# Performance work log

Measured on AMD Instinct MI355X. Metric: run time of the kernel, lower is better.

Reference implementation:

```python
import jax, jax.numpy as jnp
import numpy as np

B, P, A, V = 16, 4096, 32, 778


def _pairwise_dist(x, y):
    # x: (B, N, 3), y: (B, M, 3) -> (B, N, M) euclidean distances (torch.cdist p=2)
    d2 = (jnp.sum(x * x, -1)[:, :, None]
          + jnp.sum(y * y, -1)[:, None, :]
          - 2.0 * jnp.einsum('bnd,bmd->bnm', x, y))
    return jnp.sqrt(jnp.maximum(d2, 1e-12))


def setup_inputs() -> dict:
    key = jax.random.key(0)
    ks = jax.random.split(key, 8)
    verts = jax.random.normal(ks[0], (B, V, 3), jnp.float32) * 0.1
    anchors = jax.random.normal(ks[1], (B, A, 3), jnp.float32) * 0.1
    # choir columns: [bps_dist, dx, dy, dz, anchor_dist, anchor_idx]
    bps_d = jax.random.uniform(ks[2], (B, P, 1), jnp.float32)
    deltas = jax.random.normal(ks[3], (B, P, 3), jnp.float32) * 0.05
    anc_d = jax.random.uniform(ks[4], (B, P, 1), jnp.float32) * 0.2
    anc_i = jax.random.randint(ks[5], (B, P, 1), 0, A).astype(jnp.float32)
    choir = jnp.concatenate([bps_d, deltas, anc_d, anc_i], axis=-1)
    hand_contacts = jax.random.uniform(ks[6], (B, P), jnp.float32)
    bps_mean = jax.random.normal(ks[7], (B, 1, 3), jnp.float32) * 0.1
    bps_scalar = jnp.float32(1.5)
    # BPS basis: random uniform points in the unit ball (bps_type='random_uniform', radius=1)
    rng = np.random.default_rng(42)
    dirs = rng.standard_normal((P, 3)).astype(np.float32)
    dirs /= np.linalg.norm(dirs, axis=-1, keepdims=True)
    rad = rng.random((P, 1)).astype(np.float32) ** (1.0 / 3.0)
    bps_basis = jnp.asarray(dirs * rad)
    return {
        'verts': verts, 'anchors': anchors, 'choir': choir,
        'hand_contacts': hand_contacts, 'bps_mean': bps_mean,
        'bps_scalar': bps_scalar, 'bps_basis': bps_basis,
    }


def reference(verts, anchors, choir, hand_contacts, bps_mean, bps_scalar, bps_basis):
    # BPS decode: basis point + encoded delta -> target point cloud (B, P, 3)
    tgt_points = bps_basis[None, :, :] + choir[:, :, 1:4]
    # denormalize back to world frame
    tgt_points = tgt_points / bps_scalar + bps_mean
    # distances from every target point to every MANO anchor (B, P, A)
    anchor_distances = _pairwise_dist(tgt_points, anchors)
    # gather the single associated anchor distance per point
    idx = choir[:, :, -1].astype(jnp.int32)  # (B, P)
    d_sel = jnp.take_along_axis(anchor_distances, idx[:, :, None], axis=2)[:, :, 0]
    choir_loss = jnp.mean((d_sel - choir[:, :, -2]) ** 2)
    # hand contacts: per-BPS-point min distance to hand verts -> soft contact map
    min_d = jnp.min(_pairwise_dist(tgt_points, verts), axis=-1)  # (B, P)
    contacts = jnp.exp(-100.0 * min_d * min_d)
    hand_contact_loss = jnp.mean((hand_contacts - contacts) ** 2)
    return choir_loss, hand_contact_loss
```

## Files before the change

kernel.cpp:

```cpp
#include <hip/hip_runtime.h>
#include <hip/hip_bf16.h>

#define B_ 16
#define P_ 4096
#define A_ 32
#define V_ 778
#define NPTS (B_ * P_)

#define SPLIT 8
#define CH 98
#define VP (SPLIT * CH)
#define BLOCK 256
#define PTS_PER_BLOCK (BLOCK / SPLIT)
#define NBLOCKS (NPTS / PTS_PER_BLOCK)
#define BLOCKS_PER_B (P_ / PTS_PER_BLOCK)

__global__ __launch_bounds__(BLOCK) void dual_hoi_main_kernel(
    const float* __restrict__ verts,
    const float* __restrict__ anchors,
    const float* __restrict__ choir,
    const float* __restrict__ hand_contacts,
    const float* __restrict__ bps_mean,
    const float* __restrict__ bps_scalar,
    const float* __restrict__ bps_basis,
    float2* __restrict__ partials)
{
    __shared__ float4 sv[VP];

    const int tid = threadIdx.x;
    const int bid = blockIdx.x;
    const int b = bid / BLOCKS_PER_B;
    const int pbase = (bid % BLOCKS_PER_B) * PTS_PER_BLOCK;
    const int plocal = tid >> 3;
    const int chunk = tid & (SPLIT - 1);
    const int p = pbase + plocal;
    const int gid = (b << 12) + p;

    const float* vb = verts + b * (V_ * 3);
    for (int j = tid; j < VP; j += BLOCK) {
        sv[j] = (j < V_)
              ? make_float4(vb[3 * j], vb[3 * j + 1], vb[3 * j + 2], 0.0f)
              : make_float4(1e18f, 1e18f, 1e18f, 0.0f);
    }
    __syncthreads();

    const float inv_s = 1.0f / bps_scalar[0];
    const float* c = choir + (size_t)gid * 6;
    const float c1 = c[1], c2 = c[2], c3 = c[3];
    const float tx = (bps_basis[3 * p]     + c1) * inv_s + bps_mean[3 * b];
    const float ty = (bps_basis[3 * p + 1] + c2) * inv_s + bps_mean[3 * b + 1];
    const float tz = (bps_basis[3 * p + 2] + c3) * inv_s + bps_mean[3 * b + 2];

    const float4* pv = sv + chunk * CH;
    float m0 = 1e30f, m1 = 1e30f;
    #pragma unroll 7
    for (int j = 0; j < CH; j += 2) {
        const float4 v0 = pv[j];
        const float4 v1 = pv[j + 1];
        const float dx0 = tx - v0.x, dy0 = ty - v0.y, dz0 = tz - v0.z;
        m0 = fminf(m0, fmaf(dx0, dx0, fmaf(dy0, dy0, dz0 * dz0)));
        const float dx1 = tx - v1.x, dy1 = ty - v1.y, dz1 = tz - v1.z;
        m1 = fminf(m1, fmaf(dx1, dx1, fmaf(dy1, dy1, dz1 * dz1)));
    }
    float m = fminf(m0, m1);
    m = fminf(m, __shfl_xor(m, 1));
    m = fminf(m, __shfl_xor(m, 2));
    m = fminf(m, __shfl_xor(m, 4));

    float s1 = 0.0f, s2 = 0.0f;
    if (chunk == 0) {
        const float mind2 = fmaxf(m, 1e-12f);
        const float contact = expf(-100.0f * mind2);
        const float e2 = hand_contacts[gid] - contact;
        s2 = e2 * e2;
        const int idx = (int)c[5];
        const float* an = anchors + ((size_t)b * A_ + idx) * 3;
        const float ax = tx - an[0], ay = ty - an[1], az = tz - an[2];
        const float dsel = sqrtf(fmaxf(fmaf(ax, ax, fmaf(ay, ay, az * az)), 1e-12f));
        const float e1 = dsel - c[4];
        s1 = e1 * e1;
    }

    for (int off = 32; off > 0; off >>= 1) {
        s1 += __shfl_down(s1, off);
        s2 += __shfl_down(s2, off);
    }
    __shared__ float red[8];
    const int wave = tid >> 6;
    if ((tid & 63) == 0) { red[wave] = s1; red[4 + wave] = s2; }
    __syncthreads();
    if (tid == 0) {
        partials[bid] = make_float2(red[0] + red[1] + red[2] + red[3],
                                    red[4] + red[5] + red[6] + red[7]);
    }
}

__global__ __launch_bounds__(BLOCK) void dual_hoi_reduce_kernel(
    const float2* __restrict__ partials, float* __restrict__ out)
{
    const int tid = threadIdx.x;
    float s1 = 0.0f, s2 = 0.0f;
    #pragma unroll
    for (int i = tid; i < NBLOCKS; i += BLOCK) {
        const float2 v = partials[i];
        s1 += v.x;
        s2 += v.y;
    }
    for (int off = 32; off > 0; off >>= 1) {
        s1 += __shfl_down(s1, off);
        s2 += __shfl_down(s2, off);
    }
    __shared__ float red[8];
    const int wave = tid >> 6;
    if ((tid & 63) == 0) { red[wave] = s1; red[4 + wave] = s2; }
    __syncthreads();
    if (tid == 0) {
        out[0] = (red[0] + red[1] + red[2] + red[3]) * (1.0f / NPTS);
        out[1] = (red[4] + red[5] + red[6] + red[7]) * (1.0f / NPTS);
    }
}

extern "C" void kernel_launch(void* const* d_in, const int* in_sizes, int n_in,
                              void* d_out, int out_size, void* d_ws, size_t ws_size,
                              hipStream_t stream) {
    const float* verts         = (const float*)d_in[0];
    const float* anchors       = (const float*)d_in[1];
    const float* choir         = (const float*)d_in[2];
    const float* hand_contacts = (const float*)d_in[3];
    const float* bps_mean      = (const float*)d_in[4];
    const float* bps_scalar    = (const float*)d_in[5];
    const float* bps_basis     = (const float*)d_in[6];
    float* out = (float*)d_out;
    float2* partials = (float2*)d_ws;

    dual_hoi_main_kernel<<<NBLOCKS, BLOCK, 0, stream>>>(
        verts, anchors, choir, hand_contacts, bps_mean, bps_scalar, bps_basis,
        partials);
    dual_hoi_reduce_kernel<<<1, BLOCK, 0, stream>>>(partials, out);
}
```

Baseline: 93.89 us.

## Register-block four points per thread to reuse each LDS vertex load

Each thread now evaluates 4 target points against each vertex it reads from shared memory, so every LDS load feeds 4 distance computations instead of 1. The vertex set is split 16 ways instead of 8, and each block covers 64 points. This cuts the shared-memory bandwidth per FLOP and reduces the number of blocks, each of which repeats the vertex staging. In exchange it adds register pressure and an extra shuffle stage, and reduces the total thread count, which may lower occupancy.

```diff
diff --git a/kernel.cpp b/kernel.cpp
--- a/kernel.cpp
+++ b/kernel.cpp
@@ -7,15 +7,16 @@
 #define V_ 778
 #define NPTS (B_ * P_)
 
-#define SPLIT 8
-#define CH 98
+#define SPLIT 16
+#define K 4
+#define CH 51
 #define VP (SPLIT * CH)
 #define BLOCK 256
-#define PTS_PER_BLOCK (BLOCK / SPLIT)
+#define PTS_PER_BLOCK ((BLOCK / SPLIT) * K)
 #define NBLOCKS (NPTS / PTS_PER_BLOCK)
 #define BLOCKS_PER_B (P_ / PTS_PER_BLOCK)
 
-__global__ __launch_bounds__(BLOCK) void dual_hoi_main_kernel(
+__global__ __launch_bounds__(BLOCK, 4) void dual_hoi_main_kernel(
     const float* __restrict__ verts,
     const float* __restrict__ anchors,
     const float* __restrict__ choir,
@@ -31,10 +32,8 @@
     const int bid = blockIdx.x;
     const int b = bid / BLOCKS_PER_B;
     const int pbase = (bid % BLOCKS_PER_B) * PTS_PER_BLOCK;
-    const int plocal = tid >> 3;
+    const int plocal = tid >> 4;
     const int chunk = tid & (SPLIT - 1);
-    const int p = pbase + plocal;
-    const int gid = (b << 12) + p;
 
     const float* vb = verts + b * (V_ * 3);
     for (int j = tid; j < VP; j += BLOCK) {
@@ -45,40 +44,59 @@
     __syncthreads();
 
     const float inv_s = 1.0f / bps_scalar[0];
-    const float* c = choir + (size_t)gid * 6;
-    const float c1 = c[1], c2 = c[2], c3 = c[3];
-    const float tx = (bps_basis[3 * p]     + c1) * inv_s + bps_mean[3 * b];
-    const float ty = (bps_basis[3 * p + 1] + c2) * inv_s + bps_mean[3 * b + 1];
-    const float tz = (bps_basis[3 * p + 2] + c3) * inv_s + bps_mean[3 * b + 2];
+    const float mx = bps_mean[3 * b], my = bps_mean[3 * b + 1], mz = bps_mean[3 * b + 2];
+
+    float tx[K], ty[K], tz[K];
+    int pq[K];
+    #pragma unroll
+    for (int q = 0; q < K; ++q) {
+        const int p = pbase + plocal + 16 * q;
+        pq[q] = p;
+        const int gid = (b << 12) + p;
+        const float* c = choir + (size_t)gid * 6;
+        tx[q] = (bps_basis[3 * p]     + c[1]) * inv_s + mx;
+        ty[q] = (bps_basis[3 * p + 1] + c[2]) * inv_s + my;
+        tz[q] = (bps_basis[3 * p + 2] + c[3]) * inv_s + mz;
+    }
 
     const float4* pv = sv + chunk * CH;
-    float m0 = 1e30f, m1 = 1e30f;
-    #pragma unroll 7
-    for (int j = 0; j < CH; j += 2) {
-        const float4 v0 = pv[j];
-        const float4 v1 = pv[j + 1];
-        const float dx0 = tx - v0.x, dy0 = ty - v0.y, dz0 = tz - v0.z;
-        m0 = fminf(m0, fmaf(dx0, dx0, fmaf(dy0, dy0, dz0 * dz0)));
-        const float dx1 = tx - v1.x, dy1 = ty - v1.y, dz1 = tz - v1.z;
-        m1 = fminf(m1, fmaf(dx1, dx1, fmaf(dy1, dy1, dz1 * dz1)));
+    float mn[K] = {1e30f, 1e30f, 1e30f, 1e30f};
+    #pragma unroll 3
+    for (int j = 0; j < CH; ++j) {
+        const float4 v = pv[j];
+        #pragma unroll
+        for (int q = 0; q < K; ++q) {
+            const float dx = tx[q] - v.x;
+            const float dy = ty[q] - v.y;
+            const float dz = tz[q] - v.z;
+            mn[q] = fminf(mn[q], fmaf(dx, dx, fmaf(dy, dy, dz * dz)));
+        }
     }
-    float m = fminf(m0, m1);
-    m = fminf(m, __shfl_xor(m, 1));
-    m = fminf(m, __shfl_xor(m, 2));
-    m = fminf(m, __shfl_xor(m, 4));
+    #pragma unroll
+    for (int q = 0; q < K; ++q) {
+        mn[q] = fminf(mn[q], __shfl_xor(mn[q], 1));
+        mn[q] = fminf(mn[q], __shfl_xor(mn[q], 2));
+        mn[q] = fminf(mn[q], __shfl_xor(mn[q], 4));
+        mn[q] = fminf(mn[q], __shfl_xor(mn[q], 8));
+    }
 
     float s1 = 0.0f, s2 = 0.0f;
     if (chunk == 0) {
-        const float mind2 = fmaxf(m, 1e-12f);
-        const float contact = expf(-100.0f * mind2);
-        const float e2 = hand_contacts[gid] - contact;
-        s2 = e2 * e2;
-        const int idx = (int)c[5];
-        const float* an = anchors + ((size_t)b * A_ + idx) * 3;
-        const float ax = tx - an[0], ay = ty - an[1], az = tz - an[2];
-        const float dsel = sqrtf(fmaxf(fmaf(ax, ax, fmaf(ay, ay, az * az)), 1e-12f));
-        const float e1 = dsel - c[4];
-        s1 = e1 * e1;
+        #pragma unroll
+        for (int q = 0; q < K; ++q) {
+            const int gid = (b << 12) + pq[q];
+            const float* c = choir + (size_t)gid * 6;
+            const float mind2 = fmaxf(mn[q], 1e-12f);
+            const float contact = expf(-100.0f * mind2);
+            const float e2 = hand_contacts[gid] - contact;
+            s2 += e2 * e2;
+            const int idx = (int)c[5];
+            const float* an = anchors + ((size_t)b * A_ + idx) * 3;
+            const float ax = tx[q] - an[0], ay = ty[q] - an[1], az = tz[q] - an[2];
+            const float dsel = sqrtf(fmaxf(fmaf(ax, ax, fmaf(ay, ay, az * az)), 1e-12f));
+            const float e1 = dsel - c[4];
+            s1 += e1 * e1;
+        }
     }
 
     for (int off = 32; off > 0; off >>= 1) {
```

Result: faster. 78.34 us (-16.6%).
